# Optimization experiments

Hardware: AMD Instinct MI355X
Metric: run time of the kernel (lower is better)

The kernel has to match this reference:

```python
import jax, jax.numpy as jnp
import numpy as np

N_AGENTS, RNN_H, N_HEADS, GAT_D, EMB, SDIM = 16, 64, 4, 32, 32, 128


def setup_inputs() -> dict:
    key = jax.random.key(0)
    ks = jax.random.split(key, 16)
    xav = lambda k, shp: jax.random.normal(k, shp, jnp.float32) * (2.0 / sum(shp)) ** 0.5
    return {
        'agent_qs': jax.random.normal(ks[0], (32, 128, N_AGENTS), jnp.float32),
        'states': jax.random.normal(ks[1], (32, 128, SDIM), jnp.float32),
        'hidden_states': jax.random.normal(ks[2], (32, 128, N_AGENTS, RNN_H), jnp.float32),
        'uncertainty': jax.random.uniform(ks[3], (32, 128, 1), jnp.float32),
        'W_gat': xav(ks[4], (RNN_H, N_HEADS * GAT_D)) * 1.414,
        'att_a': xav(ks[5], (1, N_HEADS, 2 * GAT_D)) * 1.414,
        'w1s_W': xav(ks[6], (SDIM + 1, N_HEADS * EMB * GAT_D)),
        'w1s_b': jnp.zeros((N_HEADS * EMB * GAT_D,), jnp.float32),
        'b1_W': xav(ks[7], (SDIM, EMB)),
        'b1_b': jnp.zeros((EMB,), jnp.float32),
        'wf_W': xav(ks[8], (SDIM, EMB)),
        'wf_b': jnp.zeros((EMB,), jnp.float32),
        'V1_W': xav(ks[9], (SDIM, EMB)),
        'V1_b': jnp.zeros((EMB,), jnp.float32),
        'V2_W': xav(ks[10], (EMB, 1)),
        'V2_b': jnp.zeros((1,), jnp.float32),
    }


def gat(h, W_gat, att_a):
    B, n, _ = h.shape
    hp = (h @ W_gat).reshape(B, n, N_HEADS, GAT_D).transpose(0, 2, 1, 3)  # (B,H,n,d)
    a_src, a_dst = att_a[0, :, :GAT_D], att_a[0, :, GAT_D:]  # (H,d) each
    # e[b,h,i,j] = <hp_i, a_src> + <hp_j, a_dst>  (same math as concat+dot)
    src = jnp.einsum('bhnd,hd->bhn', hp, a_src)
    dst = jnp.einsum('bhnd,hd->bhn', hp, a_dst)
    e = jax.nn.leaky_relu(src[:, :, :, None] + dst[:, :, None, :], 0.2)
    attn = jax.nn.softmax(e, axis=-1)
    return jax.nn.elu(jnp.einsum('bhij,bhjd->bhid', attn, hp))  # (B,H,n,d)


def reference(agent_qs, states, hidden_states, uncertainty, W_gat, att_a,
              w1s_W, w1s_b, b1_W, b1_b, wf_W, wf_b, V1_W, V1_b, V2_W, V2_b):
    bs = agent_qs.shape[0]
    s = states.reshape(-1, SDIM)                      # (B,S)
    qs = agent_qs.reshape(-1, 1, N_AGENTS)            # (B,1,n)
    hs = hidden_states.reshape(-1, N_AGENTS, RNN_H)   # (B,n,R)
    unc = uncertainty.reshape(-1, 1)
    s_aug = jnp.concatenate([s, unc], axis=1)         # (B,S+1)

    g = gat(hs, W_gat, att_a)                         # (B,H,n,d)

    w1_state = (s_aug @ w1s_W + w1s_b).reshape(-1, N_HEADS, EMB, GAT_D)
    w1_heads = jnp.abs(jnp.einsum('bhed,bhnd->bhen', w1_state, g))  # (B,H,E,n)
    w1 = w1_heads.mean(axis=1).transpose(0, 2, 1)     # (B,n,E)

    b1 = (s @ b1_W + b1_b)[:, None, :]                # (B,1,E)
    hidden = jax.nn.elu(jnp.einsum('bin,bne->bie', qs, w1) + b1)  # (B,1,E)

    w_final = jnp.abs(s @ wf_W + wf_b)[:, :, None]    # (B,E,1)
    v = (jax.nn.relu(s @ V1_W + V1_b) @ V2_W + V2_b)[:, None, :]  # (B,1,1)
    y = jnp.einsum('bie,bej->bij', hidden, w_final) + v
    return y.reshape(bs, -1, 1)
```

## Files before the change

kernel.cpp:

```cpp
#include <hip/hip_runtime.h>
#include <hip/hip_bf16.h>
#include <math.h>


typedef __attribute__((ext_vector_type(8))) short short8;
typedef __attribute__((ext_vector_type(8))) unsigned short ushort8;
typedef __attribute__((ext_vector_type(4))) float float4v;
typedef __attribute__((ext_vector_type(4))) _Float16 half4v;

static __device__ inline unsigned short f2bf(float f) {
    unsigned int x;
    __builtin_memcpy(&x, &f, 4);
    unsigned int r = x + 0x7fffu + ((x >> 16) & 1u);
    return (unsigned short)(r >> 16);
}

static __device__ inline unsigned int cvtpk(float lo, float hi) {
    __hip_bfloat162 h = __float22bfloat162_rn(make_float2(lo, hi));
    unsigned int u;
    __builtin_memcpy(&u, &h, 4);
    return u;
}

static __device__ inline short8 pack8(float4 f0, float4 f1) {
    unsigned int u[4] = {cvtpk(f0.x, f0.y), cvtpk(f0.z, f0.w),
                         cvtpk(f1.x, f1.y), cvtpk(f1.z, f1.w)};
    short8 s;
    __builtin_memcpy(&s, u, 16);
    return s;
}

__global__ __launch_bounds__(256) void k0_prep(
    const float* __restrict__ w1s_W,
    const float* __restrict__ W_gat,
    const float* __restrict__ att_a,
    const float* __restrict__ states,
    const float* __restrict__ b1_W, const float* __restrict__ b1_b,
    const float* __restrict__ wf_W, const float* __restrict__ wf_b,
    const float* __restrict__ V1_W, const float* __restrict__ V1_b,
    const float* __restrict__ V2_W, const float* __restrict__ V2_b,
    unsigned short* __restrict__ w1sTf,
    unsigned short* __restrict__ WgTf,
    float* __restrict__ b1v, float* __restrict__ wfv,
    float* __restrict__ out)
{
    __shared__ __align__(16) char SMEM[26112];
    const int tid = threadIdx.x, bx = blockIdx.x;

    if (bx < 256) {
        unsigned short* T = (unsigned short*)SMEM;
        const int c0 = bx * 16;
        const int cc = tid & 15, kr = tid >> 4;
        #pragma unroll
        for (int t = 0; t < 8; ++t) {
            int k = t * 16 + kr;
            T[cc * 136 + k] = f2bf(w1s_W[(size_t)k * 4096 + c0 + cc]);
        }
        __syncthreads();
        const int ks = tid >> 6, q = (tid >> 4) & 3, mm = tid & 15;
        *(ushort8*)&w1sTf[(size_t)bx * 2048 + tid * 8] =
            *(const ushort8*)&T[mm * 136 + ks * 32 + q * 8];
    } else if (bx == 256) {
        unsigned short* T = (unsigned short*)SMEM;
        #pragma unroll
        for (int t = 0; t < 32; ++t) {
            int i = t * 256 + tid;
            int k = i >> 7, c = i & 127;
            T[c * 72 + k] = f2bf(W_gat[k * 128 + c]);
        }
        __syncthreads();
        #pragma unroll
        for (int t = 0; t < 4; ++t) {
            int i = t * 256 + tid;
            int nt = i >> 7, w = i & 127;
            int kh = w >> 6, q = (w >> 4) & 3, mm = w & 15;
            *(ushort8*)&WgTf[nt * 1024 + w * 8] =
                *(const ushort8*)&T[(nt * 16 + mm) * 72 + kh * 32 + q * 8];
        }
        {
            const int k = tid >> 2, h = tid & 3;
            float ss = 0.f, dd = 0.f;
            #pragma unroll
            for (int d = 0; d < 32; ++d) {
                float wv = W_gat[k * 128 + h * 32 + d];
                ss = fmaf(wv, att_a[h * 64 + d], ss);
                dd = fmaf(wv, att_a[h * 64 + 32 + d], dd);
            }
            const int base = 8192 + (k >> 5) * 512 + ((k >> 3) & 3) * 128 + (k & 7);
            WgTf[base + h * 8]       = f2bf(ss);
            WgTf[base + (4 + h) * 8] = f2bf(dd);
        }
        #pragma unroll
        for (int t = 0; t < 2; ++t) {
            int i = t * 256 + tid;
            int kh = i >> 8, q = (i >> 6) & 3, mm = 8 + ((i >> 3) & 7), j = i & 7;
            WgTf[8192 + kh * 512 + q * 128 + mm * 8 + j] = 0;
        }
    } else {
        unsigned short* WLu = (unsigned short*)SMEM;
        for (int i = tid; i < 12288; i += 256) {
            float v = (i < 4096) ? b1_W[i] : (i < 8192 ? wf_W[i - 4096] : V1_W[i - 8192]);
            int set = i >> 12, k = (i >> 5) & 127, e = i & 31;
            WLu[set * 4352 + k * 34 + e] = f2bf(v);
        }
        __syncthreads();

        const int wave = tid >> 6, lane = tid & 63, mm = lane & 15, q = lane >> 4;
        const int b0w = (bx - 257) * 64 + wave * 16;

        short8 a[4];
        #pragma unroll
        for (int ks = 0; ks < 4; ++ks) {
            const float* sp = states + (size_t)(b0w + mm) * 128 + ks * 32 + q * 8;
            a[ks] = pack8(*(const float4*)sp, *(const float4*)(sp + 4));
        }
        float4v accT[6];
        #pragma unroll
        for (int nt = 0; nt < 6; ++nt) accT[nt] = (float4v){0.f, 0.f, 0.f, 0.f};
        #pragma unroll
        for (int nt = 0; nt < 6; ++nt) {
            const int set = nt >> 1, e = (nt & 1) * 16 + mm;
            #pragma unroll
            for (int ks = 0; ks < 4; ++ks) {
                ushort8 bfu;
                #pragma unroll
                for (int j = 0; j < 8; ++j)
                    bfu[j] = WLu[set * 4352 + (ks * 32 + q * 8 + j) * 34 + e];
                short8 bf;
                __builtin_memcpy(&bf, &bfu, 16);
                accT[nt] = __builtin_amdgcn_mfma_f32_16x16x32_bf16(a[ks], bf, accT[nt], 0, 0, 0);
            }
        }
        float vsum[4] = {0.f, 0.f, 0.f, 0.f};
        #pragma unroll
        for (int p = 0; p < 2; ++p) {
            const int e = p * 16 + mm;
            const float bb1 = b1_b[e], bwf = wf_b[e], bv1 = V1_b[e], v2 = V2_W[e];
            #pragma unroll
            for (int reg = 0; reg < 4; ++reg) {
                const int row = b0w + q * 4 + reg;
                b1v[(size_t)row * 32 + e] = accT[p][reg] + bb1;
                wfv[(size_t)row * 32 + e] = fabsf(accT[2 + p][reg] + bwf);
                vsum[reg] += fmaxf(accT[4 + p][reg] + bv1, 0.f) * v2;
            }
        }
        #pragma unroll
        for (int reg = 0; reg < 4; ++reg) {
            vsum[reg] += __shfl_xor(vsum[reg], 1);
            vsum[reg] += __shfl_xor(vsum[reg], 2);
            vsum[reg] += __shfl_xor(vsum[reg], 4);
            vsum[reg] += __shfl_xor(vsum[reg], 8);
        }
        if (mm == 0) {
            #pragma unroll
            for (int reg = 0; reg < 4; ++reg)
                out[b0w + q * 4 + reg] = vsum[reg] + V2_b[0];
        }
    }
}

__global__ __launch_bounds__(256) void k1_gat(
    const float* __restrict__ hidden_states,
    const unsigned short* __restrict__ WgTf,
    unsigned short* __restrict__ g_bf)
{
    const int wave = threadIdx.x >> 6;
    const int b = blockIdx.x * 4 + wave;
    const int lane = threadIdx.x & 63, m = lane & 15, quad = lane >> 4;
    __shared__ __align__(16) float sc[4 * 320];
    float* scr = &sc[wave * 320];

    const float* hrow = hidden_states + ((size_t)b * 16 + m) * 64;
    float4 f0 = *(const float4*)(hrow + quad * 8);
    float4 f1 = *(const float4*)(hrow + quad * 8 + 4);
    short8 a0 = pack8(f0, f1);
    f0 = *(const float4*)(hrow + 32 + quad * 8);
    f1 = *(const float4*)(hrow + 32 + quad * 8 + 4);
    short8 a1 = pack8(f0, f1);

    float4v hpt[9];
    #pragma unroll
    for (int nt = 0; nt < 9; ++nt) {
        short8 bf0 = *(const short8*)&WgTf[nt * 1024 + lane * 8];
        short8 bf1 = *(const short8*)&WgTf[nt * 1024 + 512 + lane * 8];
        float4v z = (float4v){0.f, 0.f, 0.f, 0.f};
        z = __builtin_amdgcn_mfma_f32_16x16x32_bf16(a0, bf0, z, 0, 0, 0);
        z = __builtin_amdgcn_mfma_f32_16x16x32_bf16(a1, bf1, z, 0, 0, 0);
        hpt[nt] = z;
    }

    {
        float4 pr = {hpt[8][0], hpt[8][1], hpt[8][2], hpt[8][3]};
        *(float4*)&scr[m * 20 + quad * 4] = pr;
    }

    #pragma unroll
    for (int h = 0; h < 4; ++h) {
        const float src_m = scr[h * 20 + m];
        float4 pdv = *(const float4*)&scr[(4 + h) * 20 + quad * 4];
        float pd[4] = {pdv.x, pdv.y, pdv.z, pdv.w};

        float e_[4];
        #pragma unroll
        for (int jj = 0; jj < 4; ++jj) {
            float x = src_m + pd[jj];
            e_[jj] = fmaxf(x, 0.2f * x);
        }
        float mx = fmaxf(fmaxf(e_[0], e_[1]), fmaxf(e_[2], e_[3]));
        mx = fmaxf(mx, __shfl_xor(mx, 16));
        mx = fmaxf(mx, __shfl_xor(mx, 32));
        float p_[4], ssum = 0.f;
        #pragma unroll
        for (int jj = 0; jj < 4; ++jj) { p_[jj] = __expf(e_[jj] - mx); ssum += p_[jj]; }
        ssum += __shfl_xor(ssum, 16);
        ssum += __shfl_xor(ssum, 32);
        const float inv = __builtin_amdgcn_rcpf(ssum);

        half4v bfrag;
        #pragma unroll
        for (int jj = 0; jj < 4; ++jj) bfrag[jj] = (_Float16)(p_[jj] * inv);

        float4v zp[2];
        #pragma unroll
        for (int p = 0; p < 2; ++p) {
            float4v ct = hpt[2 * h + p];
            half4v afrag;
            #pragma unroll
            for (int t = 0; t < 4; ++t) afrag[t] = (_Float16)ct[t];
            float4v z = (float4v){0.f, 0.f, 0.f, 0.f};
            zp[p] = __builtin_amdgcn_mfma_f32_16x16x16f16(afrag, bfrag, z, 0, 0, 0);
        }
        unsigned int w[4];
        #pragma unroll
        for (int t = 0; t < 4; ++t) {
            float x0 = zp[0][t];
            x0 = (x0 > 0.f) ? x0 : (__expf(x0) - 1.f);
            float x1 = zp[1][t];
            x1 = (x1 > 0.f) ? x1 : (__expf(x1) - 1.f);
            w[t] = cvtpk(x0, x1);
        }
        short8 o8;
        __builtin_memcpy(&o8, w, 16);
        *(short8*)&g_bf[((size_t)b * 4 + h) * 512 + m * 32 + quad * 8] = o8;
    }
}

__global__ __launch_bounds__(256) void k2_mix(
    const float* __restrict__ states,
    const unsigned short* __restrict__ w1sTf,
    const unsigned short* __restrict__ g_bf,
    const float* __restrict__ agent_qs,
    const float* __restrict__ uncertainty,
    const float* __restrict__ w1s_W,
    const float* __restrict__ w1s_b,
    const float* __restrict__ b1v, const float* __restrict__ wfv,
    float* __restrict__ out)
{
    const int r0 = blockIdx.x * 16;
    const int eg = blockIdx.y;
    const int wave = threadIdx.x >> 6;
    const int lane = threadIdx.x & 63, m = lane & 15, quad = lane >> 4;
    __shared__ __align__(16) unsigned short Wt[2][16 * 168];

    short8 a[4];
    #pragma unroll
    for (int ks = 0; ks < 4; ++ks) {
        const float* sp = states + (size_t)(r0 + m) * 128 + ks * 32 + quad * 8;
        a[ks] = pack8(*(const float4*)sp, *(const float4*)(sp + 4));
    }
    float us[4];
    #pragma unroll
    for (int reg = 0; reg < 4; ++reg)
        us[reg] = uncertainty[r0 + quad * 4 + reg];
    float qs_r[4];
    #pragma unroll
    for (int rr = 0; rr < 4; ++rr)
        qs_r[rr] = agent_qs[(r0 + wave * 4 + rr) * 16 + m];

    const float* w128 = w1s_W + (size_t)128 * 4096;
    float Sacc[4][4] = {};

    #pragma unroll
    for (int h = 0; h < 4; ++h) {
        unsigned short* buf = &Wt[h & 1][0];

        float4v acc0, acc1;
        #pragma unroll
        for (int t = 0; t < 2; ++t) {
            const int ctl = wave * 2 + t;
            const int ct = h * 64 + eg * 8 + ctl;
            const int c_loc = ctl * 16 + m;
            const int cg = h * 1024 + eg * 128 + c_loc;
            const float wfix = w128[cg], bias = w1s_b[cg];
            float4v z = (float4v){0.f, 0.f, 0.f, 0.f};
            #pragma unroll
            for (int ks = 0; ks < 4; ++ks) {
                short8 bfr = *(const short8*)&w1sTf[(size_t)ct * 2048 + ks * 512 + lane * 8];
                z = __builtin_amdgcn_mfma_f32_16x16x32_bf16(a[ks], bfr, z, 0, 0, 0);
            }
            #pragma unroll
            for (int reg = 0; reg < 4; ++reg)
                z[reg] = z[reg] + us[reg] * wfix + bias;
            if (t == 0) acc0 = z; else acc1 = z;
        }
        #pragma unroll
        for (int reg = 0; reg < 4; ++reg) {
            const int row = quad * 4 + reg;
            unsigned int pair = cvtpk(acc0[reg], acc1[reg]);
            *(unsigned int*)&buf[row * 168 + wave * 40 + 2 * m] = pair;
        }

        short8 gf[4];
        #pragma unroll
        for (int rr = 0; rr < 4; ++rr)
            gf[rr] = *(const short8*)&g_bf[((size_t)(r0 + wave * 4 + rr) * 4 + h) * 512 + m * 32 + quad * 8];

        __syncthreads();

        #pragma unroll
        for (int rr = 0; rr < 4; ++rr) {
            const int r = wave * 4 + rr;
            short8 af = *(const short8*)&buf[r * 168 + (m & 3) * 40 + quad * 8];
            float4v z = (float4v){0.f, 0.f, 0.f, 0.f};
            z = __builtin_amdgcn_mfma_f32_16x16x32_bf16(af, gf[rr], z, 0, 0, 0);
            #pragma unroll
            for (int reg = 0; reg < 4; ++reg)
                Sacc[rr][reg] += fabsf(z[reg]);
        }
    }

    #pragma unroll
    for (int rr = 0; rr < 4; ++rr) {
        const int r = r0 + wave * 4 + rr;
        float sn[4];
        #pragma unroll
        for (int reg = 0; reg < 4; ++reg) sn[reg] = Sacc[rr][reg] * qs_r[rr];
        #pragma unroll
        for (int mask = 1; mask <= 8; mask <<= 1) {
            #pragma unroll
            for (int reg = 0; reg < 4; ++reg) sn[reg] += __shfl_xor(sn[reg], mask);
        }
        float4 b4 = *(const float4*)&b1v[(size_t)r * 32 + eg * 4];
        float4 w4 = *(const float4*)&wfv[(size_t)r * 32 + eg * 4];
        float bq[4] = {b4.x, b4.y, b4.z, b4.w};
        float wq[4] = {w4.x, w4.y, w4.z, w4.w};
        float local = 0.f;
        #pragma unroll
        for (int reg = 0; reg < 4; ++reg) {
            float hid = 0.25f * sn[reg] + bq[reg];
            hid = (hid > 0.f) ? hid : expm1f(hid);
            local = fmaf(hid, wq[reg], local);
        }
        if (lane == 0) atomicAdd(&out[r], local);
    }
}

extern "C" void kernel_launch(void* const* d_in, const int* in_sizes, int n_in,
                              void* d_out, int out_size, void* d_ws, size_t ws_size,
                              hipStream_t stream)
{
    const float* agent_qs      = (const float*)d_in[0];
    const float* states        = (const float*)d_in[1];
    const float* hidden_states = (const float*)d_in[2];
    const float* uncertainty   = (const float*)d_in[3];
    const float* W_gat         = (const float*)d_in[4];
    const float* att_a         = (const float*)d_in[5];
    const float* w1s_W         = (const float*)d_in[6];
    const float* w1s_b         = (const float*)d_in[7];
    const float* b1_W          = (const float*)d_in[8];
    const float* b1_b          = (const float*)d_in[9];
    const float* wf_W          = (const float*)d_in[10];
    const float* wf_b          = (const float*)d_in[11];
    const float* V1_W          = (const float*)d_in[12];
    const float* V1_b          = (const float*)d_in[13];
    const float* V2_W          = (const float*)d_in[14];
    const float* V2_b          = (const float*)d_in[15];

    char* w = (char*)d_ws;
    unsigned short* w1sTf   = (unsigned short*)w;  w += (size_t)524288 * 2;
    unsigned short* WgTf    = (unsigned short*)w;  w += (size_t)9216 * 2;
    unsigned short* g_bf    = (unsigned short*)w;  w += (size_t)8388608 * 2;
    float* b1v              = (float*)w;           w += (size_t)131072 * 4;
    float* wfv              = (float*)w;           w += (size_t)131072 * 4;
    float* out              = (float*)d_out;

    k0_prep<<<321, 256, 0, stream>>>(w1s_W, W_gat, att_a, states,
                                     b1_W, b1_b, wf_W, wf_b, V1_W, V1_b,
                                     V2_W, V2_b, w1sTf, WgTf, b1v, wfv, out);

    k1_gat<<<1024, 256, 0, stream>>>(hidden_states, WgTf, g_bf);

    dim3 gmix(256, 8);
    k2_mix<<<gmix, 256, 0, stream>>>(states, w1sTf, g_bf, agent_qs, uncertainty,
                                     w1s_W, w1s_b, b1v, wfv, out);
}
```

Before: 151.6 us.

## Precompute per-row mixing weights, then fuse GAT with the mixing contraction

The state-conditioned w1 GEMM moves into a separate kernel. It writes a per-row bf16 weight tensor W2, and the GAT kernel now consumes that tensor directly. The GAT output is contracted in registers instead of being written to global memory and read back. This removes the g_bf round trip, the LDS staging, the block syncs and the atomics of the old mixing kernel, and bf16 states are cached from the prep kernel. In exchange, the materialized W2 intermediate is twice the size of the old g_bf buffer, so global memory traffic may increase.

Result: faster. 130.3 us (-14.1%).

```diff
diff --git a/kernel.cpp b/kernel.cpp
--- a/kernel.cpp
+++ b/kernel.cpp
@@ -41,6 +41,7 @@
     const float* __restrict__ V2_W, const float* __restrict__ V2_b,
     unsigned short* __restrict__ w1sTf,
     unsigned short* __restrict__ WgTf,
+    unsigned short* __restrict__ Sbf,
     float* __restrict__ b1v, float* __restrict__ wfv,
     float* __restrict__ out)
 {
@@ -114,6 +115,10 @@
             const float* sp = states + (size_t)(b0w + mm) * 128 + ks * 32 + q * 8;
             a[ks] = pack8(*(const float4*)sp, *(const float4*)(sp + 4));
         }
+        #pragma unroll
+        for (int ks = 0; ks < 4; ++ks)
+            *(short8*)&Sbf[(size_t)(b0w + mm) * 128 + ks * 32 + q * 8] = a[ks];
+
         float4v accT[6];
         #pragma unroll
         for (int nt = 0; nt < 6; ++nt) accT[nt] = (float4v){0.f, 0.f, 0.f, 0.f};
@@ -159,16 +164,95 @@
     }
 }
 
-__global__ __launch_bounds__(256) void k1_gat(
+__global__ __launch_bounds__(256) void k2a_gemm(
+    const unsigned short* __restrict__ w1sTf,
+    const unsigned short* __restrict__ Sbf,
+    const float* __restrict__ uncertainty,
+    const float* __restrict__ w1s_W,
+    const float* __restrict__ w1s_b,
+    unsigned short* __restrict__ W2)
+{
+    const int bx = blockIdx.x;
+    const int rb = bx >> 4, pg = bx & 15;
+    const int wave = threadIdx.x >> 6, lane = threadIdx.x & 63;
+    const int m = lane & 15, quad = lane >> 4;
+    const int ep = pg * 4 + wave;
+    const int ct0 = ep * 4;
+
+    const float* w128 = w1s_W + (size_t)128 * 4096;
+
+    short8 A[4][4];
+    #pragma unroll
+    for (int t = 0; t < 4; ++t)
+        #pragma unroll
+        for (int ks = 0; ks < 4; ++ks)
+            A[t][ks] = *(const short8*)&w1sTf[(size_t)(ct0 + t) * 2048 + ks * 512 + lane * 8];
+
+    float wf[4][4], bb[4][4];
+    #pragma unroll
+    for (int t = 0; t < 4; ++t) {
+        float4 w4 = *(const float4*)&w128[(ct0 + t) * 16 + quad * 4];
+        float4 b4 = *(const float4*)&w1s_b[(ct0 + t) * 16 + quad * 4];
+        wf[t][0] = w4.x; wf[t][1] = w4.y; wf[t][2] = w4.z; wf[t][3] = w4.w;
+        bb[t][0] = b4.x; bb[t][1] = b4.y; bb[t][2] = b4.z; bb[t][3] = b4.w;
+    }
+
+    #pragma unroll
+    for (int c = 0; c < 4; ++c) {
+        const int r0c = rb * 64 + c * 16;
+        const float us = uncertainty[r0c + m];
+        short8 Bf[4];
+        #pragma unroll
+        for (int ks = 0; ks < 4; ++ks)
+            Bf[ks] = *(const short8*)&Sbf[(size_t)(r0c + m) * 128 + ks * 32 + quad * 8];
+
+        float4v z[4];
+        #pragma unroll
+        for (int t = 0; t < 4; ++t) z[t] = (float4v){0.f, 0.f, 0.f, 0.f};
+        #pragma unroll
+        for (int t = 0; t < 4; ++t)
+            #pragma unroll
+            for (int ks = 0; ks < 4; ++ks)
+                z[t] = __builtin_amdgcn_mfma_f32_16x16x32_bf16(A[t][ks], Bf[ks], z[t], 0, 0, 0);
+
+        #pragma unroll
+        for (int half = 0; half < 2; ++half) {
+            const int tA = half * 2, tB = half * 2 + 1;
+            unsigned int wpk[4];
+            #pragma unroll
+            for (int reg = 0; reg < 4; ++reg) {
+                float za = z[tA][reg] + us * wf[tA][reg] + bb[tA][reg];
+                float zb = z[tB][reg] + us * wf[tB][reg] + bb[tB][reg];
+                wpk[reg] = cvtpk(za, zb);
+            }
+            short8 pk;
+            __builtin_memcpy(&pk, wpk, 16);
+            const int E = ep * 2 + half;
+            const int eo = (E >> 4) * 512 + (E & 15) * 32 + quad * 8;
+            *(short8*)&W2[(size_t)(r0c + m) * 4096 + eo] = pk;
+        }
+    }
+}
+
+__global__ __launch_bounds__(256) void k1_gatmix(
     const float* __restrict__ hidden_states,
     const unsigned short* __restrict__ WgTf,
-    unsigned short* __restrict__ g_bf)
+    const unsigned short* __restrict__ W2,
+    const float* __restrict__ agent_qs,
+    const float* __restrict__ b1v, const float* __restrict__ wfv,
+    float* __restrict__ out)
 {
     const int wave = threadIdx.x >> 6;
     const int b = blockIdx.x * 4 + wave;
     const int lane = threadIdx.x & 63, m = lane & 15, quad = lane >> 4;
     __shared__ __align__(16) float sc[4 * 320];
     float* scr = &sc[wave * 320];
+
+    short8 wfr[8];
+    #pragma unroll
+    for (int i = 0; i < 8; ++i)
+        wfr[i] = *(const short8*)&W2[(size_t)b * 4096 + i * 512 + m * 32 + quad * 8];
+    const float qs_m = agent_qs[b * 16 + m];
 
     const float* hrow = hidden_states + ((size_t)b * 16 + m) * 64;
     float4 f0 = *(const float4*)(hrow + quad * 8);
@@ -194,6 +278,8 @@
         *(float4*)&scr[m * 20 + quad * 4] = pr;
     }
 
+    float Sacc[2][4] = {};
+
     #pragma unroll
     for (int h = 0; h < 4; ++h) {
         const float src_m = scr[h * 20 + m];
@@ -239,120 +325,44 @@
             x1 = (x1 > 0.f) ? x1 : (__expf(x1) - 1.f);
             w[t] = cvtpk(x0, x1);
         }
-        short8 o8;
-        __builtin_memcpy(&o8, w, 16);
-        *(short8*)&g_bf[((size_t)b * 4 + h) * 512 + m * 32 + quad * 8] = o8;
-    }
-}
-
-__global__ __launch_bounds__(256) void k2_mix(
-    const float* __restrict__ states,
-    const unsigned short* __restrict__ w1sTf,
-    const unsigned short* __restrict__ g_bf,
-    const float* __restrict__ agent_qs,
-    const float* __restrict__ uncertainty,
-    const float* __restrict__ w1s_W,
-    const float* __restrict__ w1s_b,
-    const float* __restrict__ b1v, const float* __restrict__ wfv,
-    float* __restrict__ out)
-{
-    const int r0 = blockIdx.x * 16;
-    const int eg = blockIdx.y;
-    const int wave = threadIdx.x >> 6;
-    const int lane = threadIdx.x & 63, m = lane & 15, quad = lane >> 4;
-    __shared__ __align__(16) unsigned short Wt[2][16 * 168];
-
-    short8 a[4];
-    #pragma unroll
-    for (int ks = 0; ks < 4; ++ks) {
-        const float* sp = states + (size_t)(r0 + m) * 128 + ks * 32 + quad * 8;
-        a[ks] = pack8(*(const float4*)sp, *(const float4*)(sp + 4));
-    }
-    float us[4];
-    #pragma unroll
-    for (int reg = 0; reg < 4; ++reg)
-        us[reg] = uncertainty[r0 + quad * 4 + reg];
-    float qs_r[4];
-    #pragma unroll
-    for (int rr = 0; rr < 4; ++rr)
-        qs_r[rr] = agent_qs[(r0 + wave * 4 + rr) * 16 + m];
-
-    const float* w128 = w1s_W + (size_t)128 * 4096;
-    float Sacc[4][4] = {};
-
-    #pragma unroll
-    for (int h = 0; h < 4; ++h) {
-        unsigned short* buf = &Wt[h & 1][0];
-
-        float4v acc0, acc1;
-        #pragma unroll
-        for (int t = 0; t < 2; ++t) {
-            const int ctl = wave * 2 + t;
-            const int ct = h * 64 + eg * 8 + ctl;
-            const int c_loc = ctl * 16 + m;
-            const int cg = h * 1024 + eg * 128 + c_loc;
-            const float wfix = w128[cg], bias = w1s_b[cg];
+        short8 gfrag;
+        __builtin_memcpy(&gfrag, w, 16);
+
+        #pragma unroll
+        for (int H = 0; H < 2; ++H) {
             float4v z = (float4v){0.f, 0.f, 0.f, 0.f};
-            #pragma unroll
-            for (int ks = 0; ks < 4; ++ks) {
-                short8 bfr = *(const short8*)&w1sTf[(size_t)ct * 2048 + ks * 512 + lane * 8];
-                z = __builtin_amdgcn_mfma_f32_16x16x32_bf16(a[ks], bfr, z, 0, 0, 0);
-            }
+            z = __builtin_amdgcn_mfma_f32_16x16x32_bf16(wfr[h * 2 + H], gfrag, z, 0, 0, 0);
             #pragma unroll
             for (int reg = 0; reg < 4; ++reg)
-                z[reg] = z[reg] + us[reg] * wfix + bias;
-            if (t == 0) acc0 = z; else acc1 = z;
-        }
-        #pragma unroll
-        for (int reg = 0; reg < 4; ++reg) {
-            const int row = quad * 4 + reg;
-            unsigned int pair = cvtpk(acc0[reg], acc1[reg]);
-            *(unsigned int*)&buf[row * 168 + wave * 40 + 2 * m] = pair;
-        }
-
-        short8 gf[4];
-        #pragma unroll
-        for (int rr = 0; rr < 4; ++rr)
-            gf[rr] = *(const short8*)&g_bf[((size_t)(r0 + wave * 4 + rr) * 4 + h) * 512 + m * 32 + quad * 8];
-
-        __syncthreads();
-
-        #pragma unroll
-        for (int rr = 0; rr < 4; ++rr) {
-            const int r = wave * 4 + rr;
-            short8 af = *(const short8*)&buf[r * 168 + (m & 3) * 40 + quad * 8];
-            float4v z = (float4v){0.f, 0.f, 0.f, 0.f};
-            z = __builtin_amdgcn_mfma_f32_16x16x32_bf16(af, gf[rr], z, 0, 0, 0);
-            #pragma unroll
-            for (int reg = 0; reg < 4; ++reg)
-                Sacc[rr][reg] += fabsf(z[reg]);
-        }
-    }
-
-    #pragma unroll
-    for (int rr = 0; rr < 4; ++rr) {
-        const int r = r0 + wave * 4 + rr;
+                Sacc[H][reg] += fabsf(z[reg]);
+        }
+    }
+
+    float local = 0.f;
+    #pragma unroll
+    for (int H = 0; H < 2; ++H) {
         float sn[4];
         #pragma unroll
-        for (int reg = 0; reg < 4; ++reg) sn[reg] = Sacc[rr][reg] * qs_r[rr];
+        for (int reg = 0; reg < 4; ++reg) sn[reg] = Sacc[H][reg] * qs_m;
         #pragma unroll
         for (int mask = 1; mask <= 8; mask <<= 1) {
             #pragma unroll
             for (int reg = 0; reg < 4; ++reg) sn[reg] += __shfl_xor(sn[reg], mask);
         }
-        float4 b4 = *(const float4*)&b1v[(size_t)r * 32 + eg * 4];
-        float4 w4 = *(const float4*)&wfv[(size_t)r * 32 + eg * 4];
+        float4 b4 = *(const float4*)&b1v[(size_t)b * 32 + H * 16 + quad * 4];
+        float4 w4 = *(const float4*)&wfv[(size_t)b * 32 + H * 16 + quad * 4];
         float bq[4] = {b4.x, b4.y, b4.z, b4.w};
         float wq[4] = {w4.x, w4.y, w4.z, w4.w};
-        float local = 0.f;
         #pragma unroll
         for (int reg = 0; reg < 4; ++reg) {
             float hid = 0.25f * sn[reg] + bq[reg];
             hid = (hid > 0.f) ? hid : expm1f(hid);
             local = fmaf(hid, wq[reg], local);
         }
-        if (lane == 0) atomicAdd(&out[r], local);
-    }
+    }
+    local += __shfl_xor(local, 16);
+    local += __shfl_xor(local, 32);
+    if (lane == 0) out[b] = out[b] + local;
 }
 
 extern "C" void kernel_launch(void* const* d_in, const int* in_sizes, int n_in,
@@ -379,18 +389,18 @@
     char* w = (char*)d_ws;
     unsigned short* w1sTf   = (unsigned short*)w;  w += (size_t)524288 * 2;
     unsigned short* WgTf    = (unsigned short*)w;  w += (size_t)9216 * 2;
-    unsigned short* g_bf    = (unsigned short*)w;  w += (size_t)8388608 * 2;
+    unsigned short* Sbf     = (unsigned short*)w;  w += (size_t)524288 * 2;
+    unsigned short* W2      = (unsigned short*)w;  w += (size_t)16777216 * 2;
     float* b1v              = (float*)w;           w += (size_t)131072 * 4;
     float* wfv              = (float*)w;           w += (size_t)131072 * 4;
     float* out              = (float*)d_out;
 
     k0_prep<<<321, 256, 0, stream>>>(w1s_W, W_gat, att_a, states,
                                      b1_W, b1_b, wf_W, wf_b, V1_W, V1_b,
-                                     V2_W, V2_b, w1sTf, WgTf, b1v, wfv, out);
-
-    k1_gat<<<1024, 256, 0, stream>>>(hidden_states, WgTf, g_bf);
-
-    dim3 gmix(256, 8);
-    k2_mix<<<gmix, 256, 0, stream>>>(states, w1sTf, g_bf, agent_qs, uncertainty,
-                                     w1s_W, w1s_b, b1v, wfv, out);
-}
+                                     V2_W, V2_b, w1sTf, WgTf, Sbf, b1v, wfv, out);
+
+    k2a_gemm<<<1024, 256, 0, stream>>>(w1sTf, Sbf, uncertainty, w1s_W, w1s_b, W2);
+
+    k1_gatmix<<<1024, 256, 0, stream>>>(hidden_states, WgTf, W2, agent_qs,
+                                        b1v, wfv, out);
+}
```
